# Performance work log

Measured on AMD Instinct MI355X. Metric: run time of the kernel, lower is better.

Reference implementation:

```python
import jax, jax.numpy as jnp
import numpy as np
from jax import lax

H = 50  # hidden_size


def _lstm_layer(x, w_ih, w_hh, b_ih, b_hh):
    """Single LSTM layer, batch_first input x: [B, T, I]. PyTorch gate order i,f,g,o."""
    B = x.shape[0]
    # Precompute input projections for all timesteps: [B, T, 4H]
    x_proj = jnp.einsum('bti,gi->btg', x, w_ih) + b_ih + b_hh
    xs = jnp.swapaxes(x_proj, 0, 1)  # time-major [T, B, 4H]

    def step(carry, xp):
        h, c = carry
        gates = xp + h @ w_hh.T  # [B, 4H]
        i, f, g, o = jnp.split(gates, 4, axis=-1)
        i = jax.nn.sigmoid(i)
        f = jax.nn.sigmoid(f)
        g = jnp.tanh(g)
        o = jax.nn.sigmoid(o)
        c = f * c + i * g
        h = o * jnp.tanh(c)
        return (h, c), h

    h0 = jnp.zeros((B, H), dtype=x.dtype)
    c0 = jnp.zeros((B, H), dtype=x.dtype)
    (_, _), hs = lax.scan(step, (h0, c0), xs)
    return jnp.swapaxes(hs, 0, 1)  # back to [B, T, H]


def setup_inputs() -> dict:
    key = jax.random.key(0)
    ks = jax.random.split(key, 11)
    B, T = 512, 256
    I, O = 144, 144
    s = 0.1
    return {
        'x': jax.random.normal(ks[0], (B, T, 16, 9), dtype=jnp.float32),
        'w_ih0': jax.random.normal(ks[1], (4 * H, I), dtype=jnp.float32) * s,
        'w_hh0': jax.random.normal(ks[2], (4 * H, H), dtype=jnp.float32) * s,
        'b_ih0': jax.random.normal(ks[3], (4 * H,), dtype=jnp.float32) * s,
        'b_hh0': jax.random.normal(ks[4], (4 * H,), dtype=jnp.float32) * s,
        'w_ih1': jax.random.normal(ks[5], (4 * H, H), dtype=jnp.float32) * s,
        'w_hh1': jax.random.normal(ks[6], (4 * H, H), dtype=jnp.float32) * s,
        'b_ih1': jax.random.normal(ks[7], (4 * H,), dtype=jnp.float32) * s,
        'b_hh1': jax.random.normal(ks[8], (4 * H,), dtype=jnp.float32) * s,
        'w_fc': jax.random.normal(ks[9], (O, H), dtype=jnp.float32) * s,
        'b_fc': jax.random.normal(ks[10], (O,), dtype=jnp.float32) * s,
    }


def reference(x, w_ih0, w_hh0, b_ih0, b_hh0, w_ih1, w_hh1, b_ih1, b_hh1, w_fc, b_fc):
    B, T = x.shape[0], x.shape[1]
    x = x.reshape(B, T, -1)  # [B, T, 144]
    h1 = _lstm_layer(x, w_ih0, w_hh0, b_ih0, b_hh0)   # [B, T, H]
    h2 = _lstm_layer(h1, w_ih1, w_hh1, b_ih1, b_hh1)  # [B, T, H] (dropout inactive in eval)
    last = h2[:, -1, :]                               # [B, H]
    out = last @ w_fc.T + b_fc                        # [B, 144]
    return out.reshape(-1, 16, 9)
```

## Files before the change

### kernel.cpp

```cpp
#include <hip/hip_runtime.h>
#include <hip/hip_fp16.h>
#include <cstdint>
#include <cstddef>

#define H    50
#define TT   256
#define BATCH 512
#define KDIM 144
#define ODIM 144
#define NW   32
#define WS   8

typedef _Float16 half8  __attribute__((ext_vector_type(8)));
typedef _Float16 half4v __attribute__((ext_vector_type(4)));
typedef float    floatx4 __attribute__((ext_vector_type(4)));
typedef int      int4v  __attribute__((ext_vector_type(4)));

__device__ __forceinline__ float rcpf(float x) { return __builtin_amdgcn_rcpf(x); }
__device__ __forceinline__ float sigm(float x) { return rcpf(1.0f + __expf(-x)); }
__device__ __forceinline__ float tanhx(float x) {
    return 1.0f - 2.0f * rcpf(__expf(2.0f * x) + 1.0f);
}

__device__ __forceinline__ void sync_lds() {
    asm volatile("s_waitcnt lgkmcnt(0)\n\ts_barrier" ::: "memory");
}
__device__ __forceinline__ void wave_lds_fence() {
    asm volatile("s_waitcnt lgkmcnt(0)" ::: "memory");
}

__device__ __forceinline__ half8 make_a0(const float* __restrict__ Whh0,
                                         int kkA, int gate, int q, int s) {
    const float* r0 = Whh0 + (size_t)(gate * H + (kkA < H ? kkA : 0)) * H;
    half8 r;
    #pragma unroll
    for (int j = 0; j < 8; ++j) {
        const int k = s * 32 + q * 8 + j;
        r[j] = (_Float16)((kkA < H && k < H) ? r0[k] : 0.0f);
    }
    return r;
}
__device__ __forceinline__ half8 make_ax(const float* __restrict__ Wih0,
                                         const float* __restrict__ bih0,
                                         const float* __restrict__ bhh0,
                                         int kkA, int gate, int q, int s) {
    const int p = gate * H + (kkA < H ? kkA : 0);
    half8 r;
    #pragma unroll
    for (int j = 0; j < 8; ++j) {
        const int k = s * 32 + q * 8 + j;
        float v = 0.0f;
        if (kkA < H) {
            if (k < KDIM)        v = Wih0[(size_t)p * KDIM + k];
            else if (k == KDIM)  v = bih0[p] + bhh0[p];
        }
        r[j] = (_Float16)v;
    }
    return r;
}
__device__ __forceinline__ half8 make_a1(const float* __restrict__ Wih1,
                                         const float* __restrict__ Whh1,
                                         const float* __restrict__ bih1,
                                         const float* __restrict__ bhh1,
                                         int kkA, int gate, int q, int s) {
    const int p = gate * H + (kkA < H ? kkA : 0);
    half8 r;
    #pragma unroll
    for (int j = 0; j < 8; ++j) {
        const int k = s * 32 + q * 8 + j;
        float v = 0.0f;
        if (kkA < H) {
            if (k < H)            v = Wih1[(size_t)p * H + k];
            else if (k < 2 * H)   v = Whh1[(size_t)p * H + (k - H)];
            else if (k == 100)    v = bih1[p] + bhh1[p];
        }
        r[j] = (_Float16)v;
    }
    return r;
}

__global__ __launch_bounds__(512) void wprep(const float* __restrict__ Whh0,
                                             const float* __restrict__ Wih0,
                                             const float* __restrict__ bih0,
                                             const float* __restrict__ bhh0,
                                             const float* __restrict__ Wih1,
                                             const float* __restrict__ Whh1,
                                             const float* __restrict__ bih1,
                                             const float* __restrict__ bhh1,
                                             _Float16* __restrict__ Acat) {
    const int tid  = threadIdx.x;
    const int f    = blockIdx.x;
    const int lane = tid & 63;
    const int w    = tid >> 6;
    const int prow = lane & 15;
    const int q    = lane >> 4;
    const int gate = prow & 3;
    const int kkA0 = 8 * w + 0 + (prow >> 2);
    const int kkA1 = 8 * w + 4 + (prow >> 2);
    half8 v;
    if      (f < 2)  v = make_a0(Whh0, kkA0, gate, q, f);
    else if (f < 4)  v = make_a0(Whh0, kkA1, gate, q, f - 2);
    else if (f < 9)  v = make_ax(Wih0, bih0, bhh0, kkA0, gate, q, f - 4);
    else if (f < 14) v = make_ax(Wih0, bih0, bhh0, kkA1, gate, q, f - 9);
    else if (f < 18) v = make_a1(Wih1, Whh1, bih1, bhh1, kkA0, gate, q, f - 14);
    else             v = make_a1(Wih1, Whh1, bih1, bhh1, kkA1, gate, q, f - 18);
    *(half8*)&Acat[(size_t)tid * 176 + f * 8] = v;
}

__global__ __launch_bounds__(512, 1) void lstm_fused(
    const float* __restrict__ X,
    const _Float16* __restrict__ Acat,
    const float* __restrict__ Wfc, const float* __restrict__ bfc,
    float* __restrict__ out)
{
    const int b0   = blockIdx.x * 2;
    const int tid  = threadIdx.x;
    const int lane = tid & 63;
    const int w    = tid >> 6;
    const int col  = lane & 15;
    const int q    = lane >> 4;

    __shared__ __align__(16) _Float16 B2[2][4][4][16][8];
    __shared__ __align__(16) float    scr[8][2][2][8][4];
    __shared__ __align__(16) float    gp[64 * 72];
    __shared__ __align__(16) _Float16 XB[2][5][4][16][8];
    __shared__ float h1f[2][52];

    int4v Ap[22];
    #pragma unroll
    for (int i = 0; i < 22; ++i)
        Ap[i] = __builtin_bit_cast(int4v, *(const half8*)&Acat[(size_t)tid * 176 + i * 8]);
    #pragma unroll
    for (int i = 0; i < 22; ++i) asm volatile("" : "+a"(Ap[i]));

    const bool act  = lane < 32;
    const int  aL   = (lane >> 4) & 1;
    const int  atl  = (lane >> 3) & 1;
    const int  aidx = lane & 7;
    const int  au   = 8 * w + 4 * atl + (aidx >> 1);
    const int  acol = aidx & 1;
    const int  ak   = aL * H + au;
    float c = 0.0f;

    const int cs1 = tid / 36,         kk1 = tid % 36;
    const int cs2 = (tid + 512) / 36, kk2 = (tid + 512) % 36;
    const float* xp1 = X + ((size_t)(b0 + (cs1 & 1)) * TT + (cs1 >> 1)) * KDIM + kk1 * 4;
    const float* xp2 = X + ((size_t)(b0 + (cs2 & 1)) * TT + (cs2 >> 1)) * KDIM + kk2 * 4;

    for (int i = tid; i < 2048; i += 512) ((int*)B2)[i] = 0;
    for (int i = tid; i < 2560; i += 512) ((int*)XB)[i] = 0;
    __syncthreads();
    if (tid < 4)  B2[tid >> 1][3][0][tid & 1][4]  = (_Float16)1.0f;
    if (tid < 32) XB[tid >> 4][4][2][tid & 15][0] = (_Float16)1.0f;
    {
        const float4 v1 = *(const float4*)xp1;
        const int s = kk1 >> 3, qq = (kk1 >> 1) & 3, j0 = (kk1 & 1) * 4;
        half4v h; h[0]=(_Float16)v1.x; h[1]=(_Float16)v1.y; h[2]=(_Float16)v1.z; h[3]=(_Float16)v1.w;
        *(half4v*)&XB[0][s][qq][cs1][j0] = h;
        if (tid < 64) {
            const float4 v2 = *(const float4*)xp2;
            const int s2 = kk2 >> 3, q2 = (kk2 >> 1) & 3, j2 = (kk2 & 1) * 4;
            half4v h2; h2[0]=(_Float16)v2.x; h2[1]=(_Float16)v2.y; h2[2]=(_Float16)v2.z; h2[3]=(_Float16)v2.w;
            *(half4v*)&XB[0][s2][q2][cs2][j2] = h2;
        }
    }
    __syncthreads();

    for (int W = 0; W < NW; ++W) {
        #pragma unroll
        for (int i = 0; i < 22; ++i) asm volatile("" : "+a"(Ap[i]));
        const int cb = W & 1, nb = cb ^ 1;
        const bool more = (W + 1) < NW;
        float4 xv1, xv2;
        if (more) {
            xv1 = *(const float4*)(xp1 + (size_t)(W + 1) * WS * KDIM);
            if (tid < 64) xv2 = *(const float4*)(xp2 + (size_t)(W + 1) * WS * KDIM);
        }
        {
            half8 xbf[5];
            #pragma unroll
            for (int s = 0; s < 5; ++s) xbf[s] = *(const half8*)&XB[cb][s][q][col][0];
            floatx4 px0 = (floatx4)(0.0f), px1 = (floatx4)(0.0f);
            #pragma unroll
            for (int s = 0; s < 5; ++s) {
                px0 = __builtin_amdgcn_mfma_f32_16x16x32_f16(__builtin_bit_cast(half8, Ap[4 + s]), xbf[s], px0, 0, 0, 0);
                px1 = __builtin_amdgcn_mfma_f32_16x16x32_f16(__builtin_bit_cast(half8, Ap[9 + s]), xbf[s], px1, 0, 0, 0);
            }
            const int gb = (col >> 1) * 8 + (col & 1) * 4;
            *(floatx4*)&gp[(8 * w + q) * 72 + gb]     = px0;
            *(floatx4*)&gp[(8 * w + 4 + q) * 72 + gb] = px1;
        }
        #pragma unroll
        for (int i = 0; i < WS; ++i) {
            const int rb = i & 1, wb = rb ^ 1;
            half8 bf[4];
            #pragma unroll
            for (int s = 0; s < 4; ++s) bf[s] = *(const half8*)&B2[rb][s][q][col][0];
            floatx4 a0[2], a1[2];
            #pragma unroll
            for (int tl = 0; tl < 2; ++tl) { a0[tl] = (floatx4)(0.0f); a1[tl] = (floatx4)(0.0f); }
            #pragma unroll
            for (int tl = 0; tl < 2; ++tl) {
                a0[tl] = __builtin_amdgcn_mfma_f32_16x16x32_f16(__builtin_bit_cast(half8, Ap[tl*2+0]), bf[0], a0[tl], 0, 0, 0);
                a0[tl] = __builtin_amdgcn_mfma_f32_16x16x32_f16(__builtin_bit_cast(half8, Ap[tl*2+1]), bf[1], a0[tl], 0, 0, 0);
                #pragma unroll
                for (int s = 0; s < 4; ++s)
                    a1[tl] = __builtin_amdgcn_mfma_f32_16x16x32_f16(__builtin_bit_cast(half8, Ap[14+tl*4+s]), bf[s], a1[tl], 0, 0, 0);
            }
            if (col < 2) {
                #pragma unroll
                for (int tl = 0; tl < 2; ++tl) {
                    *(floatx4*)&scr[w][0][tl][q * 2 + col][0] = a0[tl];
                    *(floatx4*)&scr[w][1][tl][q * 2 + col][0] = a1[tl];
                }
            }
            wave_lds_fence();
            if (act && (aL == 0 || W > 0 || i > 0)) {
                floatx4 g = *(const floatx4*)&scr[w][aL][atl][aidx][0];
                if (aL == 0) {
                    const floatx4 gx = *(const floatx4*)&gp[au * 72 + i * 8 + acol * 4];
                    g[0] += gx[0]; g[1] += gx[1]; g[2] += gx[2]; g[3] += gx[3];
                }
                const float gi = sigm(g[0]), gf = sigm(g[1]);
                const float gg = tanhx(g[2]), go = sigm(g[3]);
                c = gf * c + gi * gg;
                const float hv = go * tanhx(c);
                if (au < H)
                    B2[wb][ak >> 5][(ak >> 3) & 3][acol][ak & 7] = (_Float16)hv;
            }
            if (i == 3 && more) {
                {
                    const int s = kk1 >> 3, qq = (kk1 >> 1) & 3, j0 = (kk1 & 1) * 4;
                    half4v h; h[0]=(_Float16)xv1.x; h[1]=(_Float16)xv1.y; h[2]=(_Float16)xv1.z; h[3]=(_Float16)xv1.w;
                    *(half4v*)&XB[nb][s][qq][cs1][j0] = h;
                }
                if (tid < 64) {
                    const int s2 = kk2 >> 3, q2 = (kk2 >> 1) & 3, j2 = (kk2 & 1) * 4;
                    half4v h2; h2[0]=(_Float16)xv2.x; h2[1]=(_Float16)xv2.y; h2[2]=(_Float16)xv2.z; h2[3]=(_Float16)xv2.w;
                    *(half4v*)&XB[nb][s2][q2][cs2][j2] = h2;
                }
            }
            sync_lds();
        }
    }
    {
        half8 bf[4];
        #pragma unroll
        for (int s = 0; s < 4; ++s) bf[s] = *(const half8*)&B2[0][s][q][col][0];
        #pragma unroll
        for (int tl = 0; tl < 2; ++tl) {
            floatx4 a1 = (floatx4)(0.0f);
            #pragma unroll
            for (int s = 0; s < 4; ++s)
                a1 = __builtin_amdgcn_mfma_f32_16x16x32_f16(__builtin_bit_cast(half8, Ap[14+tl*4+s]), bf[s], a1, 0, 0, 0);
            if (col < 2)
                *(floatx4*)&scr[w][1][tl][q * 2 + col][0] = a1;
        }
        wave_lds_fence();
        if (act && aL == 1) {
            const floatx4 g = *(const floatx4*)&scr[w][1][atl][aidx][0];
            const float gi = sigm(g[0]), gf = sigm(g[1]);
            const float gg = tanhx(g[2]), go = sigm(g[3]);
            c = gf * c + gi * gg;
            if (au < H) h1f[acol][au] = go * tanhx(c);
        }
        sync_lds();
    }
    if (tid < 2 * ODIM) {
        const int r = tid / ODIM, o = tid - r * ODIM;
        float s = bfc[o];
        const float* wr = Wfc + (size_t)o * H;
        #pragma unroll
        for (int k = 0; k < H; ++k) s += wr[k] * h1f[r][k];
        out[(size_t)(b0 + r) * ODIM + o] = s;
    }
}

extern "C" void kernel_launch(void* const* d_in, const int* in_sizes, int n_in,
                              void* d_out, int out_size, void* d_ws, size_t ws_size,
                              hipStream_t stream) {
    const float* x    = (const float*)d_in[0];
    const float* wih0 = (const float*)d_in[1];
    const float* whh0 = (const float*)d_in[2];
    const float* bih0 = (const float*)d_in[3];
    const float* bhh0 = (const float*)d_in[4];
    const float* wih1 = (const float*)d_in[5];
    const float* whh1 = (const float*)d_in[6];
    const float* bih1 = (const float*)d_in[7];
    const float* bhh1 = (const float*)d_in[8];
    const float* wfc  = (const float*)d_in[9];
    const float* bfc  = (const float*)d_in[10];
    float* outp = (float*)d_out;

    _Float16* Acat = (_Float16*)d_ws;

    wprep<<<22, 512, 0, stream>>>(whh0, wih0, bih0, bhh0, wih1, whh1, bih1, bhh1, Acat);
    lstm_fused<<<BATCH / 2, 512, 0, stream>>>(x, Acat, wfc, bfc, outp);
}
```

Measured before the change: 259.3 us.

## Fuse weight prep into LSTM kernel and compute gates directly from MFMA registers

Removes the separate wprep launch. Each block now builds its fp16 MFMA A-fragments straight from the fp32 weights, which drops one kernel launch and the workspace round trip. The gate nonlinearities are now applied directly in the lanes that hold the MFMA accumulators (col<2). This replaces the scratch-LDS shuffle and its fence, cutting LDS traffic and latency on the serial recurrence. The cost is that activation work is spread over 4 accumulator elements per lane with more per-lane transcendentals, and every block redoes the weight conversion with scattered global loads.

```diff
diff --git a/kernel.cpp b/kernel.cpp
--- a/kernel.cpp
+++ b/kernel.cpp
@@ -25,9 +25,6 @@
 __device__ __forceinline__ void sync_lds() {
     asm volatile("s_waitcnt lgkmcnt(0)\n\ts_barrier" ::: "memory");
 }
-__device__ __forceinline__ void wave_lds_fence() {
-    asm volatile("s_waitcnt lgkmcnt(0)" ::: "memory");
-}
 
 __device__ __forceinline__ half8 make_a0(const float* __restrict__ Whh0,
                                          int kkA, int gate, int q, int s) {
@@ -79,37 +76,12 @@
     return r;
 }
 
-__global__ __launch_bounds__(512) void wprep(const float* __restrict__ Whh0,
-                                             const float* __restrict__ Wih0,
-                                             const float* __restrict__ bih0,
-                                             const float* __restrict__ bhh0,
-                                             const float* __restrict__ Wih1,
-                                             const float* __restrict__ Whh1,
-                                             const float* __restrict__ bih1,
-                                             const float* __restrict__ bhh1,
-                                             _Float16* __restrict__ Acat) {
-    const int tid  = threadIdx.x;
-    const int f    = blockIdx.x;
-    const int lane = tid & 63;
-    const int w    = tid >> 6;
-    const int prow = lane & 15;
-    const int q    = lane >> 4;
-    const int gate = prow & 3;
-    const int kkA0 = 8 * w + 0 + (prow >> 2);
-    const int kkA1 = 8 * w + 4 + (prow >> 2);
-    half8 v;
-    if      (f < 2)  v = make_a0(Whh0, kkA0, gate, q, f);
-    else if (f < 4)  v = make_a0(Whh0, kkA1, gate, q, f - 2);
-    else if (f < 9)  v = make_ax(Wih0, bih0, bhh0, kkA0, gate, q, f - 4);
-    else if (f < 14) v = make_ax(Wih0, bih0, bhh0, kkA1, gate, q, f - 9);
-    else if (f < 18) v = make_a1(Wih1, Whh1, bih1, bhh1, kkA0, gate, q, f - 14);
-    else             v = make_a1(Wih1, Whh1, bih1, bhh1, kkA1, gate, q, f - 18);
-    *(half8*)&Acat[(size_t)tid * 176 + f * 8] = v;
-}
-
 __global__ __launch_bounds__(512, 1) void lstm_fused(
     const float* __restrict__ X,
-    const _Float16* __restrict__ Acat,
+    const float* __restrict__ Whh0, const float* __restrict__ Wih0,
+    const float* __restrict__ bih0, const float* __restrict__ bhh0,
+    const float* __restrict__ Wih1, const float* __restrict__ Whh1,
+    const float* __restrict__ bih1, const float* __restrict__ bhh1,
     const float* __restrict__ Wfc, const float* __restrict__ bfc,
     float* __restrict__ out)
 {
@@ -121,26 +93,34 @@
     const int q    = lane >> 4;
 
     __shared__ __align__(16) _Float16 B2[2][4][4][16][8];
-    __shared__ __align__(16) float    scr[8][2][2][8][4];
     __shared__ __align__(16) float    gp[64 * 72];
     __shared__ __align__(16) _Float16 XB[2][5][4][16][8];
     __shared__ float h1f[2][52];
 
     int4v Ap[22];
-    #pragma unroll
-    for (int i = 0; i < 22; ++i)
-        Ap[i] = __builtin_bit_cast(int4v, *(const half8*)&Acat[(size_t)tid * 176 + i * 8]);
+    {
+        const int prow = lane & 15;
+        const int gate = prow & 3;
+        const int kkA0 = 8 * w + 0 + (prow >> 2);
+        const int kkA1 = 8 * w + 4 + (prow >> 2);
+        Ap[0] = __builtin_bit_cast(int4v, make_a0(Whh0, kkA0, gate, q, 0));
+        Ap[1] = __builtin_bit_cast(int4v, make_a0(Whh0, kkA0, gate, q, 1));
+        Ap[2] = __builtin_bit_cast(int4v, make_a0(Whh0, kkA1, gate, q, 0));
+        Ap[3] = __builtin_bit_cast(int4v, make_a0(Whh0, kkA1, gate, q, 1));
+        #pragma unroll
+        for (int s = 0; s < 5; ++s) Ap[4 + s] = __builtin_bit_cast(int4v, make_ax(Wih0, bih0, bhh0, kkA0, gate, q, s));
+        #pragma unroll
+        for (int s = 0; s < 5; ++s) Ap[9 + s] = __builtin_bit_cast(int4v, make_ax(Wih0, bih0, bhh0, kkA1, gate, q, s));
+        #pragma unroll
+        for (int s = 0; s < 4; ++s) Ap[14 + s] = __builtin_bit_cast(int4v, make_a1(Wih1, Whh1, bih1, bhh1, kkA0, gate, q, s));
+        #pragma unroll
+        for (int s = 0; s < 4; ++s) Ap[18 + s] = __builtin_bit_cast(int4v, make_a1(Wih1, Whh1, bih1, bhh1, kkA1, gate, q, s));
+    }
     #pragma unroll
     for (int i = 0; i < 22; ++i) asm volatile("" : "+a"(Ap[i]));
 
-    const bool act  = lane < 32;
-    const int  aL   = (lane >> 4) & 1;
-    const int  atl  = (lane >> 3) & 1;
-    const int  aidx = lane & 7;
-    const int  au   = 8 * w + 4 * atl + (aidx >> 1);
-    const int  acol = aidx & 1;
-    const int  ak   = aL * H + au;
-    float c = 0.0f;
+    float c0[2] = {0.0f, 0.0f};
+    float c1[2] = {0.0f, 0.0f};
 
     const int cs1 = tid / 36,         kk1 = tid % 36;
     const int cs2 = (tid + 512) / 36, kk2 = (tid + 512) % 36;
@@ -196,6 +176,11 @@
             half8 bf[4];
             #pragma unroll
             for (int s = 0; s < 4; ++s) bf[s] = *(const half8*)&B2[rb][s][q][col][0];
+            floatx4 gx0, gx1;
+            if (col < 2) {
+                gx0 = *(const floatx4*)&gp[(8 * w + q) * 72 + i * 8 + col * 4];
+                gx1 = *(const floatx4*)&gp[(8 * w + 4 + q) * 72 + i * 8 + col * 4];
+            }
             floatx4 a0[2], a1[2];
             #pragma unroll
             for (int tl = 0; tl < 2; ++tl) { a0[tl] = (floatx4)(0.0f); a1[tl] = (floatx4)(0.0f); }
@@ -210,23 +195,32 @@
             if (col < 2) {
                 #pragma unroll
                 for (int tl = 0; tl < 2; ++tl) {
-                    *(floatx4*)&scr[w][0][tl][q * 2 + col][0] = a0[tl];
-                    *(floatx4*)&scr[w][1][tl][q * 2 + col][0] = a1[tl];
-                }
-            }
-            wave_lds_fence();
-            if (act && (aL == 0 || W > 0 || i > 0)) {
-                floatx4 g = *(const floatx4*)&scr[w][aL][atl][aidx][0];
-                if (aL == 0) {
-                    const floatx4 gx = *(const floatx4*)&gp[au * 72 + i * 8 + acol * 4];
+                    const int u = 8 * w + 4 * tl + q;
+                    floatx4 g = a0[tl];
+                    const floatx4 gx = tl ? gx1 : gx0;
                     g[0] += gx[0]; g[1] += gx[1]; g[2] += gx[2]; g[3] += gx[3];
-                }
-                const float gi = sigm(g[0]), gf = sigm(g[1]);
-                const float gg = tanhx(g[2]), go = sigm(g[3]);
-                c = gf * c + gi * gg;
-                const float hv = go * tanhx(c);
-                if (au < H)
-                    B2[wb][ak >> 5][(ak >> 3) & 3][acol][ak & 7] = (_Float16)hv;
+                    const float gi = sigm(g[0]), gf = sigm(g[1]);
+                    const float gg = tanhx(g[2]), go = sigm(g[3]);
+                    c0[tl] = gf * c0[tl] + gi * gg;
+                    const float hv = go * tanhx(c0[tl]);
+                    if (u < H)
+                        B2[wb][u >> 5][(u >> 3) & 3][col][u & 7] = (_Float16)hv;
+                }
+                if (W > 0 || i > 0) {
+                    #pragma unroll
+                    for (int tl = 0; tl < 2; ++tl) {
+                        const int u = 8 * w + 4 * tl + q;
+                        const floatx4 g = a1[tl];
+                        const float gi = sigm(g[0]), gf = sigm(g[1]);
+                        const float gg = tanhx(g[2]), go = sigm(g[3]);
+                        c1[tl] = gf * c1[tl] + gi * gg;
+                        const float hv = go * tanhx(c1[tl]);
+                        if (u < H) {
+                            const int k = H + u;
+                            B2[wb][k >> 5][(k >> 3) & 3][col][k & 7] = (_Float16)hv;
+                        }
+                    }
+                }
             }
             if (i == 3 && more) {
                 {
@@ -247,22 +241,24 @@
         half8 bf[4];
         #pragma unroll
         for (int s = 0; s < 4; ++s) bf[s] = *(const half8*)&B2[0][s][q][col][0];
+        floatx4 a1[2];
         #pragma unroll
         for (int tl = 0; tl < 2; ++tl) {
-            floatx4 a1 = (floatx4)(0.0f);
+            a1[tl] = (floatx4)(0.0f);
             #pragma unroll
             for (int s = 0; s < 4; ++s)
-                a1 = __builtin_amdgcn_mfma_f32_16x16x32_f16(__builtin_bit_cast(half8, Ap[14+tl*4+s]), bf[s], a1, 0, 0, 0);
-            if (col < 2)
-                *(floatx4*)&scr[w][1][tl][q * 2 + col][0] = a1;
-        }
-        wave_lds_fence();
-        if (act && aL == 1) {
-            const floatx4 g = *(const floatx4*)&scr[w][1][atl][aidx][0];
-            const float gi = sigm(g[0]), gf = sigm(g[1]);
-            const float gg = tanhx(g[2]), go = sigm(g[3]);
-            c = gf * c + gi * gg;
-            if (au < H) h1f[acol][au] = go * tanhx(c);
+                a1[tl] = __builtin_amdgcn_mfma_f32_16x16x32_f16(__builtin_bit_cast(half8, Ap[14+tl*4+s]), bf[s], a1[tl], 0, 0, 0);
+        }
+        if (col < 2) {
+            #pragma unroll
+            for (int tl = 0; tl < 2; ++tl) {
+                const int u = 8 * w + 4 * tl + q;
+                const floatx4 g = a1[tl];
+                const float gi = sigm(g[0]), gf = sigm(g[1]);
+                const float gg = tanhx(g[2]), go = sigm(g[3]);
+                c1[tl] = gf * c1[tl] + gi * gg;
+                if (u < H) h1f[col][u] = go * tanhx(c1[tl]);
+            }
         }
         sync_lds();
     }
@@ -292,8 +288,7 @@
     const float* bfc  = (const float*)d_in[10];
     float* outp = (float*)d_out;
 
-    _Float16* Acat = (_Float16*)d_ws;
-
-    wprep<<<22, 512, 0, stream>>>(whh0, wih0, bih0, bhh0, wih1, whh1, bih1, bhh1, Acat);
-    lstm_fused<<<BATCH / 2, 512, 0, stream>>>(x, Acat, wfc, bfc, outp);
-}
+    lstm_fused<<<BATCH / 2, 512, 0, stream>>>(x, whh0, wih0, bih0, bhh0,
+                                              wih1, whh1, bih1, bhh1,
+                                              wfc, bfc, outp);
+}
```

Result: slower. 352.0 us (+35.7%).
